# Performance work log

Measured on AMD Instinct MI355X. Metric: run time of the kernel, lower is better.

The kernel has to match this reference:

```python
import jax, jax.numpy as jnp
import numpy as np


def _conv(x, k, pad):
    # x: [B,1,H,W], k: [1,1,kh,kw]
    return jax.lax.conv_general_dilated(
        x, k, window_strides=(1, 1), padding=[(pad, pad), (pad, pad)],
        dimension_numbers=('NCHW', 'OIHW', 'NCHW'))


def _gauss_kernel(size=15, sigma=2.0):
    c = np.arange(size, dtype=np.float32) - size // 2
    k = np.exp(-(c[:, None] ** 2 + c[None, :] ** 2) / (2.0 * sigma ** 2))
    k = k / k.sum()
    return jnp.asarray(k, dtype=jnp.float32)[None, None]


_SOBEL_X = jnp.array([[[[-1., 0., 1.], [-2., 0., 2.], [-1., 0., 1.]]]], dtype=jnp.float32)
_SOBEL_Y = jnp.array([[[[-1., -2., -1.], [0., 0., 0.], [1., 2., 1.]]]], dtype=jnp.float32)
_GAUSS = _gauss_kernel(15, 2.0)


def _edge_density(img):
    gray = 0.299 * img[:, 0] + 0.587 * img[:, 1] + 0.114 * img[:, 2]  # [B,H,W]
    box = jnp.ones((1, 1, 5, 5), jnp.float32) / 25.0  # avg_pool2d, count_include_pad
    blurred = _conv(gray[:, None], box, 2)
    gx = _conv(blurred, _SOBEL_X, 1)
    gy = _conv(blurred, _SOBEL_Y, 1)
    mag = jnp.sqrt(gx ** 2 + gy ** 2)
    hi = mag.max() * 0.2
    lo = hi * 0.3
    edge_map = ((mag > lo) & (mag < hi)).astype(jnp.float32)
    return _conv(edge_map, _GAUSS, 7)  # [B,1,H,W]


def _color_sparsity(img):
    # Replaces the O(K*B*H*W) python loop over unique quantized colors with a
    # 32^3-bin histogram (scatter-add) and a single per-pixel gather.
    b, c, h, w = img.shape
    idx = jnp.clip(jnp.round(img * 31.0), 0, 31).astype(jnp.int32)  # [B,3,H,W]
    code = idx[:, 0] * 1024 + idx[:, 1] * 32 + idx[:, 2]  # [B,H,W]
    counts = jnp.zeros(32 * 32 * 32, jnp.float32).at[code.reshape(-1)].add(1.0)
    prob = counts[code] / float(b * h * w)  # [B,H,W]
    return (-jnp.log(prob + 1e-9) * 1.5)[:, None]  # [B,1,H,W]


def setup_inputs() -> dict:
    key = jax.random.key(0)
    img = jax.random.uniform(key, (1, 3, 3072, 3072), dtype=jnp.float32)
    return {
        'img': img,
        'alpha': jnp.asarray(0.5, dtype=jnp.float32),
        'beta': jnp.asarray(0.5, dtype=jnp.float32),
    }


def reference(img, alpha, beta):
    ed = _edge_density(img)
    cs = _color_sparsity(img)
    en = (ed - ed.min()) / (ed.max() - ed.min() + 1e-9)
    cn = (cs - cs.min()) / (cs.max() - cs.min() + 1e-9)
    return jax.nn.sigmoid(alpha * en + beta * cn)  # [B,1,H,W]
```

## Files before the change

kernel.cpp:

```cpp
#include <hip/hip_runtime.h>
#include <math.h>

#define TW 3072
#define TH 3072
#define NPIX (TW*TH)

__device__ __forceinline__ int qcode(float r, float g, float b) {
    int ir = min(max((int)rintf(__fmul_rn(r, 31.f)), 0), 31);
    int ig = min(max((int)rintf(__fmul_rn(g, 31.f)), 0), 31);
    int ib = min(max((int)rintf(__fmul_rn(b, 31.f)), 0), 31);
    return ir * 1024 + ig * 32 + ib;
}

__device__ __forceinline__ float grayf(float r, float g, float b) {
    return __fadd_rn(__fadd_rn(__fmul_rn(0.299f, r), __fmul_rn(0.587f, g)),
                     __fmul_rn(0.114f, b));
}

__global__ __launch_bounds__(1024) void k_pre(const float4* __restrict__ img4,
                                              float4* __restrict__ gray4,
                                              ushort4* __restrict__ code4,
                                              unsigned* __restrict__ parthist,
                                              unsigned* __restrict__ scal) {
    if (blockIdx.x == 0 && threadIdx.x == 0) {
        scal[0] = 0u;
        scal[1] = 0x7F800000u;
        scal[2] = 0u;
        scal[3] = 0u;
        scal[4] = 0xFFFFFFFFu;
    }
    __shared__ unsigned lh[16384];
    for (int t = threadIdx.x; t < 16384; t += 1024) lh[t] = 0u;
    __syncthreads();
    const int total4 = NPIX / 4;
    const int stride = 512 * 1024;
    int base = blockIdx.x * 1024 + threadIdx.x;
#pragma unroll
    for (int k = 0; k < 4; k += 2) {
        int p = base + k * stride;
        int q = p + stride;
        float4 r0 = img4[p], g0 = img4[p + total4], b0 = img4[p + 2 * total4];
        float4 r1 = img4[q], g1 = img4[q + total4], b1 = img4[q + 2 * total4];
        float4 gy0, gy1;
        gy0.x = grayf(r0.x, g0.x, b0.x); gy0.y = grayf(r0.y, g0.y, b0.y);
        gy0.z = grayf(r0.z, g0.z, b0.z); gy0.w = grayf(r0.w, g0.w, b0.w);
        gy1.x = grayf(r1.x, g1.x, b1.x); gy1.y = grayf(r1.y, g1.y, b1.y);
        gy1.z = grayf(r1.z, g1.z, b1.z); gy1.w = grayf(r1.w, g1.w, b1.w);
        gray4[p] = gy0;
        gray4[q] = gy1;
        int c0 = qcode(r0.x, g0.x, b0.x), c1 = qcode(r0.y, g0.y, b0.y);
        int c2 = qcode(r0.z, g0.z, b0.z), c3 = qcode(r0.w, g0.w, b0.w);
        int d0 = qcode(r1.x, g1.x, b1.x), d1 = qcode(r1.y, g1.y, b1.y);
        int d2 = qcode(r1.z, g1.z, b1.z), d3 = qcode(r1.w, g1.w, b1.w);
        atomicAdd(&lh[c0 >> 1], (c0 & 1) ? 0x10000u : 1u);
        atomicAdd(&lh[c1 >> 1], (c1 & 1) ? 0x10000u : 1u);
        atomicAdd(&lh[c2 >> 1], (c2 & 1) ? 0x10000u : 1u);
        atomicAdd(&lh[c3 >> 1], (c3 & 1) ? 0x10000u : 1u);
        atomicAdd(&lh[d0 >> 1], (d0 & 1) ? 0x10000u : 1u);
        atomicAdd(&lh[d1 >> 1], (d1 & 1) ? 0x10000u : 1u);
        atomicAdd(&lh[d2 >> 1], (d2 & 1) ? 0x10000u : 1u);
        atomicAdd(&lh[d3 >> 1], (d3 & 1) ? 0x10000u : 1u);
        ushort4 cc, dd;
        cc.x = (unsigned short)c0; cc.y = (unsigned short)c1;
        cc.z = (unsigned short)c2; cc.w = (unsigned short)c3;
        dd.x = (unsigned short)d0; dd.y = (unsigned short)d1;
        dd.z = (unsigned short)d2; dd.w = (unsigned short)d3;
        code4[p] = cc;
        code4[q] = dd;
    }
    {
        int p = base + 4 * stride;
        if (p < total4) {
            float4 r = img4[p], g = img4[p + total4], b = img4[p + 2 * total4];
            float4 gy;
            gy.x = grayf(r.x, g.x, b.x); gy.y = grayf(r.y, g.y, b.y);
            gy.z = grayf(r.z, g.z, b.z); gy.w = grayf(r.w, g.w, b.w);
            gray4[p] = gy;
            int c0 = qcode(r.x, g.x, b.x), c1 = qcode(r.y, g.y, b.y);
            int c2 = qcode(r.z, g.z, b.z), c3 = qcode(r.w, g.w, b.w);
            atomicAdd(&lh[c0 >> 1], (c0 & 1) ? 0x10000u : 1u);
            atomicAdd(&lh[c1 >> 1], (c1 & 1) ? 0x10000u : 1u);
            atomicAdd(&lh[c2 >> 1], (c2 & 1) ? 0x10000u : 1u);
            atomicAdd(&lh[c3 >> 1], (c3 & 1) ? 0x10000u : 1u);
            ushort4 cc;
            cc.x = (unsigned short)c0; cc.y = (unsigned short)c1;
            cc.z = (unsigned short)c2; cc.w = (unsigned short)c3;
            code4[p] = cc;
        }
    }
    __syncthreads();
    unsigned* dst = parthist + (size_t)blockIdx.x * 16384;
    for (int t = threadIdx.x; t < 16384; t += 1024) dst[t] = lh[t];
}

__global__ __launch_bounds__(1024) void k_reduce(const unsigned* __restrict__ parthist,
                                                 float* __restrict__ cstab,
                                                 unsigned* __restrict__ scal) {
    __shared__ unsigned slo[1024], shi[1024];
    int tid = threadIdx.x;
    int tsub = tid >> 6;
    int pl = tid & 63;
    int b = blockIdx.x * 64 + pl;
    unsigned lo = 0u, hi = 0u;
#pragma unroll 8
    for (int j = 0; j < 32; j++) {
        unsigned v = parthist[(size_t)(tsub * 32 + j) * 16384 + b];
        lo += v & 0xFFFFu;
        hi += v >> 16;
    }
    slo[tid] = lo;
    shi[tid] = hi;
    __syncthreads();
    if (tid < 64) {
        unsigned Lo = 0u, Hi = 0u;
#pragma unroll
        for (int t = 0; t < 16; t++) { Lo += slo[t * 64 + tid]; Hi += shi[t * 64 + tid]; }
        const float N = (float)NPIX;
        int bb = blockIdx.x * 64 + tid;
        cstab[2 * bb]     = -logf((float)Lo / N + 1e-9f) * 1.5f;
        cstab[2 * bb + 1] = -logf((float)Hi / N + 1e-9f) * 1.5f;
        unsigned mx = max(Lo, Hi);
        unsigned mn = 0xFFFFFFFFu;
        if (Lo) mn = Lo;
        if (Hi) mn = min(mn, Hi);
#pragma unroll
        for (int o = 32; o > 0; o >>= 1) {
            mx = max(mx, (unsigned)__shfl_down((int)mx, o));
            mn = min(mn, (unsigned)__shfl_down((int)mn, o));
        }
        if (tid == 0) { atomicMax(&scal[3], mx); atomicMin(&scal[4], mn); }
    }
}

__device__ __forceinline__ void blockMaxMinAtomic(float vmax, float vmin,
                                                  unsigned* pmax, unsigned* pmin) {
#pragma unroll
    for (int o = 32; o > 0; o >>= 1) {
        vmax = fmaxf(vmax, __shfl_down(vmax, o));
        vmin = fminf(vmin, __shfl_down(vmin, o));
    }
    __shared__ float smax[8], smin[8];
    int lane = threadIdx.x & 63, wv = threadIdx.x >> 6;
    if (lane == 0) { smax[wv] = vmax; smin[wv] = vmin; }
    __syncthreads();
    if (threadIdx.x == 0) {
        int nw = blockDim.x >> 6;
        float a = smax[0], b = smin[0];
        for (int k = 1; k < nw; k++) { a = fmaxf(a, smax[k]); b = fminf(b, smin[k]); }
        if (pmax) atomicMax(pmax, __float_as_uint(a));
        if (pmin) atomicMin(pmin, __float_as_uint(b));
    }
}

#define BS_W 256
#define BS_H 16
#define GTW 264
#define GTH 22
#define BLW 260
#define BLH 18
__global__ __launch_bounds__(512, 6) void k_boxsobel(const float* __restrict__ g,
                                                     float* __restrict__ mag,
                                                     unsigned* __restrict__ scal) {
    __shared__ float GT[GTH * GTW];
    __shared__ float BL[BLH * BLW];
    int tid = threadIdx.x;
    int x0 = blockIdx.x * BS_W;
    int y0 = blockIdx.y * BS_H;
    for (int t = tid; t < GTH * GTW; t += 512) {
        int ly = t / GTW, lx = t - ly * GTW;
        int y = y0 - 3 + ly, x = x0 - 3 + lx;
        GT[t] = ((unsigned)y < TH && (unsigned)x < TW) ? g[(size_t)y * TW + x] : 0.f;
    }
    __syncthreads();
    for (int t = tid; t < BLH * 65; t += 512) {
        int by = t / 65, gx = t - by * 65;
        int c0 = gx * 4;
        float acc[4] = {0.f, 0.f, 0.f, 0.f};
#pragma unroll
        for (int a = 0; a < 5; a++) {
            const float* rp = &GT[(by + a) * GTW + c0];
            float4 A = *(const float4*)rp;
            float4 B = *(const float4*)(rp + 4);
            float v[8] = {A.x, A.y, A.z, A.w, B.x, B.y, B.z, B.w};
#pragma unroll
            for (int j = 0; j < 4; j++)
#pragma unroll
                for (int b = 0; b < 5; b++)
                    acc[j] = __fadd_rn(acc[j], __fmul_rn(v[j + b], 0.04f));
        }
        int yb = y0 - 1 + by;
        float4 o;
        float* ov = (float*)&o;
#pragma unroll
        for (int j = 0; j < 4; j++) {
            int xb = x0 - 1 + c0 + j;
            ov[j] = ((unsigned)yb < TH && (unsigned)xb < TW) ? acc[j] : 0.f;
        }
        *(float4*)&BL[by * BLW + c0] = o;
    }
    __syncthreads();
    float tmax = 0.f;
    for (int t = tid; t < BS_H * 64; t += 512) {
        int oy = t >> 6, gx = t & 63;
        int c0 = gx * 4;
        float v[3][6];
#pragma unroll
        for (int a = 0; a < 3; a++) {
            const float* rp = &BL[(oy + a) * BLW + c0];
            float4 P = *(const float4*)rp;
            float2 Q = *(const float2*)(rp + 4);
            v[a][0] = P.x; v[a][1] = P.y; v[a][2] = P.z; v[a][3] = P.w;
            v[a][4] = Q.x; v[a][5] = Q.y;
        }
        float4 mo;
        float* mv = (float*)&mo;
#pragma unroll
        for (int j = 0; j < 4; j++) {
            float gxv = 0.f;
            gxv = __fadd_rn(gxv, __fmul_rn(-1.f, v[0][j + 0]));
            gxv = __fadd_rn(gxv, v[0][j + 2]);
            gxv = __fadd_rn(gxv, __fmul_rn(-2.f, v[1][j + 0]));
            gxv = __fadd_rn(gxv, __fmul_rn(2.f, v[1][j + 2]));
            gxv = __fadd_rn(gxv, __fmul_rn(-1.f, v[2][j + 0]));
            gxv = __fadd_rn(gxv, v[2][j + 2]);
            float gyv = 0.f;
            gyv = __fadd_rn(gyv, __fmul_rn(-1.f, v[0][j + 0]));
            gyv = __fadd_rn(gyv, __fmul_rn(-2.f, v[0][j + 1]));
            gyv = __fadd_rn(gyv, __fmul_rn(-1.f, v[0][j + 2]));
            gyv = __fadd_rn(gyv, v[2][j + 0]);
            gyv = __fadd_rn(gyv, __fmul_rn(2.f, v[2][j + 1]));
            gyv = __fadd_rn(gyv, v[2][j + 2]);
            float m = sqrtf(__fadd_rn(__fmul_rn(gxv, gxv), __fmul_rn(gyv, gyv)));
            mv[j] = m;
            tmax = fmaxf(tmax, m);
        }
        *(float4*)&mag[(size_t)(y0 + oy) * TW + x0 + c0] = mo;
    }
    blockMaxMinAtomic(tmax, 0.f, &scal[0], nullptr);
}

#define GS_W 256
#define GS_H 32
#define E_H 46
#define EWB 10
__global__ __launch_bounds__(512, 6) void k_gauss(const float* __restrict__ mag,
                                                  float* __restrict__ ed,
                                                  const unsigned* __restrict__ scal,
                                                  unsigned* __restrict__ scalw) {
    __shared__ float wt[15];
    __shared__ unsigned E8[E_H * EWB];
    __shared__ float EH[E_H * GS_W];
    if (threadIdx.x == 0) {
        float w[15];
        float s = 0.f;
        for (int t = 0; t < 15; t++) {
            int c = t - 7;
            w[t] = expf(-(float)(c * c) * 0.125f);
            s += w[t];
        }
        for (int t = 0; t < 15; t++) wt[t] = w[t] / s;
    }
    __syncthreads();
    float magmax = __uint_as_float(scal[0]);
    float hi = __fmul_rn(magmax, 0.2f);
    float lo = __fmul_rn(hi, 0.3f);
    int tid = threadIdx.x;
    int lane = tid & 63, wave = tid >> 6;
    int x0 = blockIdx.x * GS_W;
    int y0 = blockIdx.y * GS_H;
    for (int item = wave; item < E_H * 5; item += 8) {
        int ly = item / 5, ch = item - ly * 5;
        int y = y0 - 7 + ly;
        int lx = ch * 64 + lane;
        int x = x0 - 7 + lx;
        float m = ((unsigned)y < TH && lx < 270 && (unsigned)x < TW)
                      ? mag[(size_t)y * TW + x] : 0.f;
        unsigned long long mask = __ballot(m > lo && m < hi);
        if (lane < 2) E8[ly * EWB + ch * 2 + lane] = (unsigned)(mask >> (32 * lane));
    }
    __syncthreads();
    for (int t = tid; t < E_H * 64; t += 512) {
        int ly = t >> 6, gx = t & 63;
        int c0 = gx * 4;
        int w0 = c0 >> 5, sh = c0 & 31;
        unsigned lo32 = E8[ly * EWB + w0];
        unsigned hi32 = E8[ly * EWB + w0 + 1];
        unsigned long long win = (((unsigned long long)hi32 << 32) | lo32) >> sh;
        float e[18];
#pragma unroll
        for (int j = 0; j < 18; j++) e[j] = (float)((unsigned)(win >> j) & 1u);
        float4 o;
        float* ov = (float*)&o;
#pragma unroll
        for (int j = 0; j < 4; j++) {
            float acc = 0.f;
#pragma unroll
            for (int k = 0; k < 15; k++) acc = fmaf(e[j + k], wt[k], acc);
            ov[j] = acc;
        }
        *(float4*)&EH[ly * GS_W + c0] = o;
    }
    __syncthreads();
    float tmin = INFINITY, tmax = 0.f;
    for (int t = tid; t < GS_H * 64; t += 512) {
        int r = t >> 6, gx = t & 63;
        int c0 = gx * 4;
        float a0 = 0.f, a1 = 0.f, a2 = 0.f, a3 = 0.f;
#pragma unroll
        for (int k = 0; k < 15; k++) {
            float4 v = *(const float4*)&EH[(r + k) * GS_W + c0];
            a0 = fmaf(v.x, wt[k], a0);
            a1 = fmaf(v.y, wt[k], a1);
            a2 = fmaf(v.z, wt[k], a2);
            a3 = fmaf(v.w, wt[k], a3);
        }
        float4 o; o.x = a0; o.y = a1; o.z = a2; o.w = a3;
        *(float4*)&ed[(size_t)(y0 + r) * TW + x0 + c0] = o;
        tmin = fminf(tmin, fminf(fminf(a0, a1), fminf(a2, a3)));
        tmax = fmaxf(tmax, fmaxf(fmaxf(a0, a1), fmaxf(a2, a3)));
    }
    blockMaxMinAtomic(tmax, tmin, &scalw[2], &scalw[1]);
}

__global__ __launch_bounds__(1024) void k_final(float4* __restrict__ io4,
                                                const ushort4* __restrict__ code4,
                                                const float* __restrict__ cstab,
                                                const unsigned* __restrict__ scal,
                                                const float* __restrict__ alphap,
                                                const float* __restrict__ betap) {
    __shared__ unsigned short cnS[32768];
    const float N = (float)NPIX;
    float csmin = -logf((float)scal[3] / N + 1e-9f) * 1.5f;
    float csmax = -logf((float)scal[4] / N + 1e-9f) * 1.5f;
    float csrange = csmax - csmin + 1e-9f;
    for (int t = threadIdx.x; t < 32768; t += 1024) {
        float cn = (cstab[t] - csmin) / csrange;
        int q = (int)rintf(cn * 65535.f);
        cnS[t] = (unsigned short)min(max(q, 0), 65535);
    }
    float edmin = __uint_as_float(scal[1]);
    float edmax = __uint_as_float(scal[2]);
    float edrange = edmax - edmin + 1e-9f;
    float alpha = *alphap, beta = *betap;
    __syncthreads();
    const int total4 = NPIX / 4;
    int stride = gridDim.x * blockDim.x;
    for (int p = blockIdx.x * blockDim.x + threadIdx.x; p < total4; p += stride) {
        float4 edv4 = io4[p];
        ushort4 cc = code4[p];
        float edv[4] = {edv4.x, edv4.y, edv4.z, edv4.w};
        unsigned short cv[4] = {cc.x, cc.y, cc.z, cc.w};
        float ov[4];
#pragma unroll
        for (int t = 0; t < 4; t++) {
            float en = (edv[t] - edmin) / edrange;
            float cn = (float)cnS[cv[t]] * (1.f / 65535.f);
            float x = alpha * en + beta * cn;
            ov[t] = 1.f / (1.f + expf(-x));
        }
        float4 o;
        o.x = ov[0]; o.y = ov[1]; o.z = ov[2]; o.w = ov[3];
        io4[p] = o;
    }
}

extern "C" void kernel_launch(void* const* d_in, const int* in_sizes, int n_in,
                              void* d_out, int out_size, void* d_ws, size_t ws_size,
                              hipStream_t stream) {
    const float* img = (const float*)d_in[0];
    const float* alphap = (const float*)d_in[1];
    const float* betap = (const float*)d_in[2];
    float* out = (float*)d_out;

    char* ws = (char*)d_ws;
    unsigned* scal = (unsigned*)ws;
    float* cstab = (float*)(ws + 1024 + 131072);
    float* G = (float*)(ws + 524288);
    float* M = (float*)(ws + 524288 + (size_t)NPIX * 4);
    unsigned short* code = (unsigned short*)(ws + 524288 + (size_t)NPIX * 8);
    unsigned* parthist = (unsigned*)M;

    hipLaunchKernelGGL(k_pre, dim3(512), dim3(1024), 0, stream,
                       (const float4*)img, (float4*)G, (ushort4*)code, parthist, scal);
    hipLaunchKernelGGL(k_reduce, dim3(256), dim3(1024), 0, stream, parthist, cstab, scal);
    hipLaunchKernelGGL(k_boxsobel, dim3(TW / BS_W, TH / BS_H), dim3(512), 0, stream,
                       G, M, scal);
    hipLaunchKernelGGL(k_gauss, dim3(TW / GS_W, TH / GS_H), dim3(512), 0, stream,
                       M, out, scal, scal);
    hipLaunchKernelGGL(k_final, dim3(512), dim3(1024), 0, stream, (float4*)out,
                       (const ushort4*)code, cstab, scal, alphap, betap);
}
```

Baseline: 329.2 us.

## Split preprocessing into gray/code kernel and separate histogram kernel

The fused preprocessing kernel, which ran 512 blocks of 1024 threads holding a 64KB shared histogram, is split in two. A lightweight kernel with many small blocks computes gray and the quantized codes without LDS. A second kernel then reads the 16-bit codes back and builds 256 partial histograms, so the reduction loop now sums 256 partials instead of 512. This is meant to raise occupancy and memory throughput of the streaming pass and halve the partial-histogram traffic, at the cost of an extra kernel launch and re-reading the code buffer.

```diff
diff --git a/kernel.cpp b/kernel.cpp
--- a/kernel.cpp
+++ b/kernel.cpp
@@ -17,10 +17,9 @@
                      __fmul_rn(0.114f, b));
 }
 
-__global__ __launch_bounds__(1024) void k_pre(const float4* __restrict__ img4,
+__global__ __launch_bounds__(256) void k_gray(const float4* __restrict__ img4,
                                               float4* __restrict__ gray4,
                                               ushort4* __restrict__ code4,
-                                              unsigned* __restrict__ parthist,
                                               unsigned* __restrict__ scal) {
     if (blockIdx.x == 0 && threadIdx.x == 0) {
         scal[0] = 0u;
@@ -29,16 +28,13 @@
         scal[3] = 0u;
         scal[4] = 0xFFFFFFFFu;
     }
-    __shared__ unsigned lh[16384];
-    for (int t = threadIdx.x; t < 16384; t += 1024) lh[t] = 0u;
-    __syncthreads();
     const int total4 = NPIX / 4;
-    const int stride = 512 * 1024;
-    int base = blockIdx.x * 1024 + threadIdx.x;
+    const int gstride = 2304 * 256;
+    int t0 = blockIdx.x * 256 + threadIdx.x;
 #pragma unroll
     for (int k = 0; k < 4; k += 2) {
-        int p = base + k * stride;
-        int q = p + stride;
+        int p = t0 + k * gstride;
+        int q = p + gstride;
         float4 r0 = img4[p], g0 = img4[p + total4], b0 = img4[p + 2 * total4];
         float4 r1 = img4[q], g1 = img4[q + total4], b1 = img4[q + 2 * total4];
         float4 gy0, gy1;
@@ -52,14 +48,6 @@
         int c2 = qcode(r0.z, g0.z, b0.z), c3 = qcode(r0.w, g0.w, b0.w);
         int d0 = qcode(r1.x, g1.x, b1.x), d1 = qcode(r1.y, g1.y, b1.y);
         int d2 = qcode(r1.z, g1.z, b1.z), d3 = qcode(r1.w, g1.w, b1.w);
-        atomicAdd(&lh[c0 >> 1], (c0 & 1) ? 0x10000u : 1u);
-        atomicAdd(&lh[c1 >> 1], (c1 & 1) ? 0x10000u : 1u);
-        atomicAdd(&lh[c2 >> 1], (c2 & 1) ? 0x10000u : 1u);
-        atomicAdd(&lh[c3 >> 1], (c3 & 1) ? 0x10000u : 1u);
-        atomicAdd(&lh[d0 >> 1], (d0 & 1) ? 0x10000u : 1u);
-        atomicAdd(&lh[d1 >> 1], (d1 & 1) ? 0x10000u : 1u);
-        atomicAdd(&lh[d2 >> 1], (d2 & 1) ? 0x10000u : 1u);
-        atomicAdd(&lh[d3 >> 1], (d3 & 1) ? 0x10000u : 1u);
         ushort4 cc, dd;
         cc.x = (unsigned short)c0; cc.y = (unsigned short)c1;
         cc.z = (unsigned short)c2; cc.w = (unsigned short)c3;
@@ -68,25 +56,30 @@
         code4[p] = cc;
         code4[q] = dd;
     }
-    {
-        int p = base + 4 * stride;
-        if (p < total4) {
-            float4 r = img4[p], g = img4[p + total4], b = img4[p + 2 * total4];
-            float4 gy;
-            gy.x = grayf(r.x, g.x, b.x); gy.y = grayf(r.y, g.y, b.y);
-            gy.z = grayf(r.z, g.z, b.z); gy.w = grayf(r.w, g.w, b.w);
-            gray4[p] = gy;
-            int c0 = qcode(r.x, g.x, b.x), c1 = qcode(r.y, g.y, b.y);
-            int c2 = qcode(r.z, g.z, b.z), c3 = qcode(r.w, g.w, b.w);
-            atomicAdd(&lh[c0 >> 1], (c0 & 1) ? 0x10000u : 1u);
-            atomicAdd(&lh[c1 >> 1], (c1 & 1) ? 0x10000u : 1u);
-            atomicAdd(&lh[c2 >> 1], (c2 & 1) ? 0x10000u : 1u);
-            atomicAdd(&lh[c3 >> 1], (c3 & 1) ? 0x10000u : 1u);
-            ushort4 cc;
-            cc.x = (unsigned short)c0; cc.y = (unsigned short)c1;
-            cc.z = (unsigned short)c2; cc.w = (unsigned short)c3;
-            code4[p] = cc;
-        }
+}
+
+__global__ __launch_bounds__(1024) void k_hist(const uint4* __restrict__ codeq,
+                                               unsigned* __restrict__ parthist) {
+    __shared__ unsigned lh[16384];
+    for (int t = threadIdx.x; t < 16384; t += 1024) lh[t] = 0u;
+    __syncthreads();
+    const int nchunk = NPIX / 8;
+    const int tstride = 256 * 1024;
+    for (int i = blockIdx.x * 1024 + threadIdx.x; i < nchunk; i += tstride) {
+        uint4 w = codeq[i];
+        unsigned v;
+        v = w.x;
+        { unsigned c = v & 0xFFFFu; atomicAdd(&lh[c >> 1], (c & 1) ? 0x10000u : 1u); }
+        { unsigned c = v >> 16;     atomicAdd(&lh[c >> 1], (c & 1) ? 0x10000u : 1u); }
+        v = w.y;
+        { unsigned c = v & 0xFFFFu; atomicAdd(&lh[c >> 1], (c & 1) ? 0x10000u : 1u); }
+        { unsigned c = v >> 16;     atomicAdd(&lh[c >> 1], (c & 1) ? 0x10000u : 1u); }
+        v = w.z;
+        { unsigned c = v & 0xFFFFu; atomicAdd(&lh[c >> 1], (c & 1) ? 0x10000u : 1u); }
+        { unsigned c = v >> 16;     atomicAdd(&lh[c >> 1], (c & 1) ? 0x10000u : 1u); }
+        v = w.w;
+        { unsigned c = v & 0xFFFFu; atomicAdd(&lh[c >> 1], (c & 1) ? 0x10000u : 1u); }
+        { unsigned c = v >> 16;     atomicAdd(&lh[c >> 1], (c & 1) ? 0x10000u : 1u); }
     }
     __syncthreads();
     unsigned* dst = parthist + (size_t)blockIdx.x * 16384;
@@ -102,9 +95,9 @@
     int pl = tid & 63;
     int b = blockIdx.x * 64 + pl;
     unsigned lo = 0u, hi = 0u;
-#pragma unroll 8
-    for (int j = 0; j < 32; j++) {
-        unsigned v = parthist[(size_t)(tsub * 32 + j) * 16384 + b];
+#pragma unroll
+    for (int j = 0; j < 16; j++) {
+        unsigned v = parthist[(size_t)(tsub * 16 + j) * 16384 + b];
         lo += v & 0xFFFFu;
         hi += v >> 16;
     }
@@ -380,8 +373,10 @@
     unsigned short* code = (unsigned short*)(ws + 524288 + (size_t)NPIX * 8);
     unsigned* parthist = (unsigned*)M;
 
-    hipLaunchKernelGGL(k_pre, dim3(512), dim3(1024), 0, stream,
-                       (const float4*)img, (float4*)G, (ushort4*)code, parthist, scal);
+    hipLaunchKernelGGL(k_gray, dim3(2304), dim3(256), 0, stream,
+                       (const float4*)img, (float4*)G, (ushort4*)code, scal);
+    hipLaunchKernelGGL(k_hist, dim3(256), dim3(1024), 0, stream,
+                       (const uint4*)code, parthist);
     hipLaunchKernelGGL(k_reduce, dim3(256), dim3(1024), 0, stream, parthist, cstab, scal);
     hipLaunchKernelGGL(k_boxsobel, dim3(TW / BS_W, TH / BS_H), dim3(512), 0, stream,
                        G, M, scal);
```

After: 326.6 us. Within noise of the previous version (-0.8%).

## Enlarge stencil tiles, halve histogram blocks, batch global loads for MLP

Applied to the files above, without the earlier changes.

The pre-pass now runs 256 blocks that each cover twice as many pixels, so fewer partial histograms are written and the reduce kernel sums 16 partials per slice instead of 32. The box/Sobel and Gaussian kernels use taller row tiles (24 and 48 rows) to cut the relative halo overhead. Their tile-load loops now issue all global loads into registers before the shared-memory stores or ballots, to raise memory-level parallelism. The cost is more shared memory and registers per block, fewer resident blocks (the min-blocks hint is removed), and fewer blocks in the pre-pass to fill the GPU.

```diff
diff --git a/kernel.cpp b/kernel.cpp
--- a/kernel.cpp
+++ b/kernel.cpp
@@ -33,10 +33,10 @@
     for (int t = threadIdx.x; t < 16384; t += 1024) lh[t] = 0u;
     __syncthreads();
     const int total4 = NPIX / 4;
-    const int stride = 512 * 1024;
+    const int stride = 256 * 1024;
     int base = blockIdx.x * 1024 + threadIdx.x;
 #pragma unroll
-    for (int k = 0; k < 4; k += 2) {
+    for (int k = 0; k < 8; k += 2) {
         int p = base + k * stride;
         int q = p + stride;
         float4 r0 = img4[p], g0 = img4[p + total4], b0 = img4[p + 2 * total4];
@@ -69,24 +69,22 @@
         code4[q] = dd;
     }
     {
-        int p = base + 4 * stride;
-        if (p < total4) {
-            float4 r = img4[p], g = img4[p + total4], b = img4[p + 2 * total4];
-            float4 gy;
-            gy.x = grayf(r.x, g.x, b.x); gy.y = grayf(r.y, g.y, b.y);
-            gy.z = grayf(r.z, g.z, b.z); gy.w = grayf(r.w, g.w, b.w);
-            gray4[p] = gy;
-            int c0 = qcode(r.x, g.x, b.x), c1 = qcode(r.y, g.y, b.y);
-            int c2 = qcode(r.z, g.z, b.z), c3 = qcode(r.w, g.w, b.w);
-            atomicAdd(&lh[c0 >> 1], (c0 & 1) ? 0x10000u : 1u);
-            atomicAdd(&lh[c1 >> 1], (c1 & 1) ? 0x10000u : 1u);
-            atomicAdd(&lh[c2 >> 1], (c2 & 1) ? 0x10000u : 1u);
-            atomicAdd(&lh[c3 >> 1], (c3 & 1) ? 0x10000u : 1u);
-            ushort4 cc;
-            cc.x = (unsigned short)c0; cc.y = (unsigned short)c1;
-            cc.z = (unsigned short)c2; cc.w = (unsigned short)c3;
-            code4[p] = cc;
-        }
+        int p = base + 8 * stride;
+        float4 r = img4[p], g = img4[p + total4], b = img4[p + 2 * total4];
+        float4 gy;
+        gy.x = grayf(r.x, g.x, b.x); gy.y = grayf(r.y, g.y, b.y);
+        gy.z = grayf(r.z, g.z, b.z); gy.w = grayf(r.w, g.w, b.w);
+        gray4[p] = gy;
+        int c0 = qcode(r.x, g.x, b.x), c1 = qcode(r.y, g.y, b.y);
+        int c2 = qcode(r.z, g.z, b.z), c3 = qcode(r.w, g.w, b.w);
+        atomicAdd(&lh[c0 >> 1], (c0 & 1) ? 0x10000u : 1u);
+        atomicAdd(&lh[c1 >> 1], (c1 & 1) ? 0x10000u : 1u);
+        atomicAdd(&lh[c2 >> 1], (c2 & 1) ? 0x10000u : 1u);
+        atomicAdd(&lh[c3 >> 1], (c3 & 1) ? 0x10000u : 1u);
+        ushort4 cc;
+        cc.x = (unsigned short)c0; cc.y = (unsigned short)c1;
+        cc.z = (unsigned short)c2; cc.w = (unsigned short)c3;
+        code4[p] = cc;
     }
     __syncthreads();
     unsigned* dst = parthist + (size_t)blockIdx.x * 16384;
@@ -102,9 +100,9 @@
     int pl = tid & 63;
     int b = blockIdx.x * 64 + pl;
     unsigned lo = 0u, hi = 0u;
-#pragma unroll 8
-    for (int j = 0; j < 32; j++) {
-        unsigned v = parthist[(size_t)(tsub * 32 + j) * 16384 + b];
+#pragma unroll
+    for (int j = 0; j < 16; j++) {
+        unsigned v = parthist[(size_t)(tsub * 16 + j) * 16384 + b];
         lo += v & 0xFFFFu;
         hi += v >> 16;
     }
@@ -153,23 +151,34 @@
 }
 
 #define BS_W 256
-#define BS_H 16
+#define BS_H 24
 #define GTW 264
-#define GTH 22
+#define GTH 30
 #define BLW 260
-#define BLH 18
-__global__ __launch_bounds__(512, 6) void k_boxsobel(const float* __restrict__ g,
-                                                     float* __restrict__ mag,
-                                                     unsigned* __restrict__ scal) {
+#define BLH 26
+__global__ __launch_bounds__(512) void k_boxsobel(const float* __restrict__ g,
+                                                  float* __restrict__ mag,
+                                                  unsigned* __restrict__ scal) {
     __shared__ float GT[GTH * GTW];
     __shared__ float BL[BLH * BLW];
     int tid = threadIdx.x;
     int x0 = blockIdx.x * BS_W;
     int y0 = blockIdx.y * BS_H;
-    for (int t = tid; t < GTH * GTW; t += 512) {
-        int ly = t / GTW, lx = t - ly * GTW;
-        int y = y0 - 3 + ly, x = x0 - 3 + lx;
-        GT[t] = ((unsigned)y < TH && (unsigned)x < TW) ? g[(size_t)y * TW + x] : 0.f;
+    {
+        float tmp[16];
+#pragma unroll
+        for (int u = 0; u < 16; u++) {
+            int t = tid + u * 512;
+            int ly = t / GTW, lx = t - ly * GTW;
+            int y = y0 - 3 + ly, x = x0 - 3 + lx;
+            bool in = (t < GTH * GTW) && ((unsigned)y < TH) && ((unsigned)x < TW);
+            tmp[u] = in ? g[(size_t)y * TW + x] : 0.f;
+        }
+#pragma unroll
+        for (int u = 0; u < 16; u++) {
+            int t = tid + u * 512;
+            if (t < GTH * GTW) GT[t] = tmp[u];
+        }
     }
     __syncthreads();
     for (int t = tid; t < BLH * 65; t += 512) {
@@ -240,13 +249,13 @@
 }
 
 #define GS_W 256
-#define GS_H 32
-#define E_H 46
+#define GS_H 48
+#define E_H 62
 #define EWB 10
-__global__ __launch_bounds__(512, 6) void k_gauss(const float* __restrict__ mag,
-                                                  float* __restrict__ ed,
-                                                  const unsigned* __restrict__ scal,
-                                                  unsigned* __restrict__ scalw) {
+__global__ __launch_bounds__(512) void k_gauss(const float* __restrict__ mag,
+                                               float* __restrict__ ed,
+                                               const unsigned* __restrict__ scal,
+                                               unsigned* __restrict__ scalw) {
     __shared__ float wt[15];
     __shared__ unsigned E8[E_H * EWB];
     __shared__ float EH[E_H * GS_W];
@@ -268,15 +277,25 @@
     int lane = tid & 63, wave = tid >> 6;
     int x0 = blockIdx.x * GS_W;
     int y0 = blockIdx.y * GS_H;
-    for (int item = wave; item < E_H * 5; item += 8) {
-        int ly = item / 5, ch = item - ly * 5;
-        int y = y0 - 7 + ly;
-        int lx = ch * 64 + lane;
-        int x = x0 - 7 + lx;
-        float m = ((unsigned)y < TH && lx < 270 && (unsigned)x < TW)
-                      ? mag[(size_t)y * TW + x] : 0.f;
-        unsigned long long mask = __ballot(m > lo && m < hi);
-        if (lane < 2) E8[ly * EWB + ch * 2 + lane] = (unsigned)(mask >> (32 * lane));
+    for (int item0 = wave * 5; item0 < E_H * 5; item0 += 40) {
+        float mv5[5];
+#pragma unroll
+        for (int u = 0; u < 5; u++) {
+            int item = item0 + u;
+            int ly = item / 5, ch = item - ly * 5;
+            int y = y0 - 7 + ly;
+            int lx = ch * 64 + lane;
+            int x = x0 - 7 + lx;
+            mv5[u] = ((unsigned)y < TH && lx < 270 && (unsigned)x < TW)
+                         ? mag[(size_t)y * TW + x] : 0.f;
+        }
+#pragma unroll
+        for (int u = 0; u < 5; u++) {
+            int item = item0 + u;
+            int ly = item / 5, ch = item - ly * 5;
+            unsigned long long mask = __ballot(mv5[u] > lo && mv5[u] < hi);
+            if (lane < 2) E8[ly * EWB + ch * 2 + lane] = (unsigned)(mask >> (32 * lane));
+        }
     }
     __syncthreads();
     for (int t = tid; t < E_H * 64; t += 512) {
@@ -380,7 +399,7 @@
     unsigned short* code = (unsigned short*)(ws + 524288 + (size_t)NPIX * 8);
     unsigned* parthist = (unsigned*)M;
 
-    hipLaunchKernelGGL(k_pre, dim3(512), dim3(1024), 0, stream,
+    hipLaunchKernelGGL(k_pre, dim3(256), dim3(1024), 0, stream,
                        (const float4*)img, (float4*)G, (ushort4*)code, parthist, scal);
     hipLaunchKernelGGL(k_reduce, dim3(256), dim3(1024), 0, stream, parthist, cstab, scal);
     hipLaunchKernelGGL(k_boxsobel, dim3(TW / BS_W, TH / BS_H), dim3(512), 0, stream,
```

Measured after the change: 293.1 us. 11.0% less time.
